# Optimization experiments

Hardware: AMD Instinct MI355X
Metric: run time of the kernel (lower is better)

## Reference

```python
import jax, jax.numpy as jnp
import numpy as np

H = 12        # num attention heads
W = 256       # one-sided window (attention_window // 2)
NEG = -1e9    # additive mask value


def setup_inputs() -> dict:
    key = jax.random.key(0)
    ks = jax.random.split(key, 6)
    B, S, D = 2, 4096, 768
    inp = {
        "hidden_states": jax.random.normal(ks[0], (B, S, D), dtype=jnp.float32),
        "attention_mask": jnp.zeros((B, S), dtype=jnp.float32),
        "Wq": jax.random.normal(ks[1], (D, D), dtype=jnp.float32) * 0.02,
        "bq": jnp.zeros((D,), dtype=jnp.float32),
        "Wk": jax.random.normal(ks[2], (D, D), dtype=jnp.float32) * 0.02,
        "bk": jnp.zeros((D,), dtype=jnp.float32),
        "Wv": jax.random.normal(ks[3], (D, D), dtype=jnp.float32) * 0.02,
        "bv": jnp.zeros((D,), dtype=jnp.float32),
        "Wo": jax.random.normal(ks[4], (D, D), dtype=jnp.float32) * 0.02,
        "bo": jnp.zeros((D,), dtype=jnp.float32),
    }
    return inp


def _sliding_window_attn(hidden_states, attention_mask, Wq, bq, Wk, bk, Wv, bv, Wo, bo):
    B, S, D = hidden_states.shape
    dh = D // H
    b = W                 # chunk size == one-sided window
    nb = S // b           # number of chunks (S must be multiple of W)

    # projections; Longformer scales the query by 1/sqrt(d_head)
    q = (hidden_states @ Wq.T + bq) / jnp.sqrt(jnp.float32(dh))
    k = hidden_states @ Wk.T + bk
    v = hidden_states @ Wv.T + bv

    # [B, H, S, dh]
    q = q.reshape(B, S, H, dh).transpose(0, 2, 1, 3)
    k = k.reshape(B, S, H, dh).transpose(0, 2, 1, 3)
    v = v.reshape(B, S, H, dh).transpose(0, 2, 1, 3)

    # chunk queries: [B, H, nb, b, dh]
    qb = q.reshape(B, H, nb, b, dh)

    # pad K/V by one chunk on each side, gather 3 consecutive chunks per query chunk
    kp = jnp.pad(k, ((0, 0), (0, 0), (b, b), (0, 0)))
    vp = jnp.pad(v, ((0, 0), (0, 0), (b, b), (0, 0)))
    idx = jnp.arange(nb)[:, None] * b + jnp.arange(3 * b)[None, :]  # [nb, 3b] into padded seq
    kw = kp[:, :, idx]  # [B, H, nb, 3b, dh]
    vw = vp[:, :, idx]  # [B, H, nb, 3b, dh]

    # banded scores: [B, H, nb, b, 3b]
    scores = jnp.einsum("bhnqd,bhnkd->bhnqk", qb, kw)

    # band mask: query at local pos qi (global n*b+qi) vs key at local pos ki
    # (global n*b + ki - b); relative offset = ki - b - qi, keep |offset| <= W
    rel = jnp.arange(3 * b)[None, :] - b - jnp.arange(b)[:, None]      # [b, 3b]
    band = jnp.abs(rel) <= W
    # sequence-boundary mask: key global position must lie in [0, S)
    kpos = idx - b                                                      # [nb, 3b]
    inbounds = (kpos >= 0) & (kpos < S)
    valid = band[None, :, :] & inbounds[:, None, :]                     # [nb, b, 3b]

    # key padding bias from attention_mask (wrapper passes attention_mask * -1)
    neg_mask = attention_mask * -1.0                                    # [B, S]
    mp = jnp.pad(neg_mask, ((0, 0), (b, b)))
    key_bias = mp[:, idx]                                               # [B, nb, 3b]

    scores = scores + key_bias[:, None, :, None, :]
    scores = jnp.where(valid[None, None], scores, NEG)

    probs = jax.nn.softmax(scores, axis=-1)
    ctx = jnp.einsum("bhnqk,bhnkd->bhnqd", probs, vw)                   # [B, H, nb, b, dh]
    ctx = ctx.reshape(B, H, S, dh).transpose(0, 2, 1, 3).reshape(B, S, D)

    return ctx @ Wo.T + bo


def reference(hidden_states, attention_mask, Wq, bq, Wk, bk, Wv, bv, Wo, bo):
    return _sliding_window_attn(hidden_states, attention_mask,
                                Wq, bq, Wk, bk, Wv, bv, Wo, bo)
```

## Files before the change

kernel.cpp:

```cpp
#include <hip/hip_runtime.h>
#include <hip/hip_bf16.h>
#include <stdint.h>

#define NH 12
#define DH 64
#define SEQ 4096
#define DM 768
#define NEGV -1e9f
#define LOG2E 1.4426950408889634f
#define QSCALE 0.1803368801111601f

using bf16x8 = __attribute__((ext_vector_type(8))) short;
using f32x4  = __attribute__((ext_vector_type(4))) float;

static __device__ __forceinline__ short f2bf(float f) {
  unsigned u = __builtin_bit_cast(unsigned, f);
  u += 0x7fffu + ((u >> 16) & 1u);
  return (short)(u >> 16);
}

static __device__ __forceinline__ unsigned pack2bf_rnd(float lo, float hi) {
  unsigned a = __builtin_bit_cast(unsigned, lo) + 0x8000u;
  unsigned b = __builtin_bit_cast(unsigned, hi) + 0x8000u;
  return __builtin_amdgcn_perm(b, a, 0x07060302u);
}

static __device__ __forceinline__ void gload16(const void* g, void* l) {
  __builtin_amdgcn_global_load_lds(
      (const __attribute__((address_space(1))) unsigned*)g,
      (__attribute__((address_space(3))) unsigned*)l, 16, 0, 0);
}

static __device__ __forceinline__ f32x4 mfma16(bf16x8 a, bf16x8 b, f32x4 c) {
  return __builtin_amdgcn_mfma_f32_16x16x32_bf16(a, b, c, 0, 0, 0);
}

#define SBAR() __builtin_amdgcn_sched_barrier(0)
#define WAIT8() asm volatile("s_waitcnt vmcnt(8)" ::: "memory")
#define WAIT0() asm volatile("s_waitcnt vmcnt(0)" ::: "memory")
#define HBAR() __builtin_amdgcn_s_barrier()

__global__ __launch_bounds__(256) void cvt_all(
    const float* __restrict__ X, short* __restrict__ Xb,
    const float* __restrict__ Wq, const float* __restrict__ Wk,
    const float* __restrict__ Wv, const float* __restrict__ Wo,
    short* __restrict__ Wqkv, short* __restrict__ Wob) {
  int i = blockIdx.x * 256 + threadIdx.x;
  const int nx = 8192 * 768 / 4;
  if (i < nx) {
    float4 v = ((const float4*)X)[i];
    short4 o; o.x = f2bf(v.x); o.y = f2bf(v.y); o.z = f2bf(v.z); o.w = f2bf(v.w);
    ((short4*)Xb)[i] = o;
    return;
  }
  i -= nx;
  const int n1 = 2304 * 768 / 4;
  if (i < n1) {
    int e = i * 4;
    int row = e / 768;
    const float* src;
    float sc = 1.0f;
    if (row < 768)       { src = Wq + e; sc = QSCALE; }
    else if (row < 1536) { src = Wk + e - 768 * 768; }
    else                 { src = Wv + e - 1536 * 768; }
    float4 v = *(const float4*)src;
    short4 o; o.x = f2bf(v.x * sc); o.y = f2bf(v.y * sc);
    o.z = f2bf(v.z * sc); o.w = f2bf(v.w * sc);
    ((short4*)Wqkv)[i] = o;
  } else {
    int j = i - n1;
    if (j >= 768 * 768 / 4) return;
    float4 v = ((const float4*)Wo)[j];
    short4 o; o.x = f2bf(v.x); o.y = f2bf(v.y); o.z = f2bf(v.z); o.w = f2bf(v.w);
    ((short4*)Wob)[j] = o;
  }
}

#define GEMM_PIPELINE(SM, AG, BG, ACC, LANE, WR, WC)                           \
  {                                                                            \
    const int l15 = (LANE) & 15, gw = (LANE) >> 4;                             \
    const int s_ = (l15 >> 1) & 3;                                             \
    const int NT = 12;                                             \
    auto stage = [&](int t) {                                                  \
      short* ab = (SM) + ((t & 1) << 13);                                      \
      short* bb = (SM) + 16384 + ((t & 1) << 13);                              \
      int kt = t << 6;                                                         \
      gload16((AG) + kt, ab + ldst);                                           \
      gload16((AG) + kt + 32 * 768, ab + ldst + 2048);                         \
      gload16((AG) + kt + 64 * 768, ab + ldst + 4096);                         \
      gload16((AG) + kt + 96 * 768, ab + ldst + 6144);                         \
      gload16((BG) + kt, bb + ldst);                                           \
      gload16((BG) + kt + 32 * 768, bb + ldst + 2048);                         \
      gload16((BG) + kt + 64 * 768, bb + ldst + 4096);                         \
      gload16((BG) + kt + 96 * 768, bb + ldst + 6144);                         \
    };                                                                         \
    auto compute = [&](int t) {                                                \
      const short* ab = (SM) + ((t & 1) << 13);                                \
      const short* bb = (SM) + 16384 + ((t & 1) << 13);                        \
      _Pragma("unroll") for (int kk = 0; kk < 2; ++kk) {                       \
        const int fc = (((kk << 2) + (gw ^ s_)) << 3);                         \
        bf16x8 af[4], bf[4];                                                   \
        _Pragma("unroll") for (int mi = 0; mi < 4; ++mi)                       \
            af[mi] = *(const bf16x8*)(ab + ((WR) + mi * 16 + l15) * 64 + fc);  \
        _Pragma("unroll") for (int ni = 0; ni < 4; ++ni)                       \
            bf[ni] = *(const bf16x8*)(bb + ((WC) + ni * 16 + l15) * 64 + fc);  \
        __builtin_amdgcn_s_setprio(1);                                         \
        _Pragma("unroll") for (int mi = 0; mi < 4; ++mi)                       \
            _Pragma("unroll") for (int ni = 0; ni < 4; ++ni)                   \
                ACC[mi][ni] = mfma16(af[mi], bf[ni], ACC[mi][ni]);             \
        __builtin_amdgcn_s_setprio(0);                                         \
      }                                                                        \
    };                                                                         \
    stage(0); stage(1);                                                        \
    SBAR();                                                                    \
    _Pragma("unroll 1") for (int i = 0; i < NT; ++i) {                         \
      SBAR();                                                                  \
      if (i < NT - 1) { WAIT8(); } else { WAIT0(); }                           \
      HBAR(); SBAR();                                                          \
      compute(i);                                                              \
      SBAR(); HBAR();                                                          \
      if (i + 2 < NT) stage(i + 2);                                            \
    }                                                                          \
  }

__global__ __launch_bounds__(256) void gemm_qkv(
    const short* __restrict__ Xb, const short* __restrict__ Wqkv,
    const float* __restrict__ bq, const float* __restrict__ bk,
    const float* __restrict__ bv,
    short* __restrict__ qO, short* __restrict__ kO, short* __restrict__ vT) {
  __shared__ __align__(16) short sm[32768];
  const int tid = threadIdx.x, lane = tid & 63, wid = tid >> 6;
  const int xcd = blockIdx.x & 7, kk = blockIdx.x >> 3;
  const int m0 = (xcd * 8 + (kk & 7)) * 128;
  const int n0 = (kk >> 3) * 128;
  const int wr = (wid >> 1) * 64, wc = (wid & 1) * 64;
  const int srow = tid >> 3;
  const int scol = (((tid & 7) ^ ((tid >> 4) & 3)) << 3);
  const short* Ag = Xb + (m0 + srow) * 768 + scol;
  const short* Bg = Wqkv + (n0 + srow) * 768 + scol;
  const int ldst = tid * 8;

  const int src = n0 / 768;
  const int nloc = n0 % 768;
  float bias[4];
#pragma unroll
  for (int ni = 0; ni < 4; ++ni) {
    int c = nloc + wc + ni * 16 + (lane & 15);
    bias[ni] = (src == 0) ? bq[c] * QSCALE : (src == 1) ? bk[c] : bv[c];
  }
  WAIT0(); SBAR();

  f32x4 acc[4][4] = {};
  GEMM_PIPELINE(sm, Ag, Bg, acc, lane, wr, wc);

  const int bb = m0 >> 12;
  const int s0 = m0 & (SEQ - 1);
  __syncthreads();
  if (src < 2) {
#pragma unroll
    for (int mi = 0; mi < 4; ++mi)
#pragma unroll
      for (int ni = 0; ni < 4; ++ni) {
        int row = wr + mi * 16 + ((lane >> 4) << 2);
        int col = wc + ni * 16 + (lane & 15);
#pragma unroll
        for (int r = 0; r < 4; ++r)
          sm[(row + r) * 132 + col] = f2bf(acc[mi][ni][r] + bias[ni]);
      }
    __syncthreads();
    short* dst = (src == 0) ? qO : kO;
    for (int u = tid; u < 8192; u += 256) {
      int r = u >> 6, cp = (u & 63) << 1;
      unsigned val = *(const unsigned*)&sm[r * 132 + cp];
      int c = nloc + cp;
      int h = c >> 6, d = c & 63;
      *(unsigned*)&dst[(((bb * NH + h) * SEQ) + s0 + r) * DH + d] = val;
    }
  } else {
#pragma unroll
    for (int mi = 0; mi < 4; ++mi)
#pragma unroll
      for (int ni = 0; ni < 4; ++ni) {
        int row = wr + mi * 16 + ((lane >> 4) << 2);
        int col = wc + ni * 16 + (lane & 15);
        short4 pk;
        pk.x = f2bf(acc[mi][ni][0] + bias[ni]);
        pk.y = f2bf(acc[mi][ni][1] + bias[ni]);
        pk.z = f2bf(acc[mi][ni][2] + bias[ni]);
        pk.w = f2bf(acc[mi][ni][3] + bias[ni]);
        *(short4*)&sm[col * 132 + row] = pk;
      }
    __syncthreads();
    for (int u = tid; u < 8192; u += 256) {
      int cc = u >> 6, rp = (u & 63) << 1;
      unsigned val = *(const unsigned*)&sm[cc * 132 + rp];
      int c = nloc + cc;
      int h = c >> 6, d = c & 63;
      *(unsigned*)&vT[(((bb * NH + h) * DH) + d) * SEQ + s0 + rp] = val;
    }
  }
}

__global__ __launch_bounds__(512, 4) void attn(
    const short* __restrict__ qI, const short* __restrict__ kI,
    const short* __restrict__ vT, const float* __restrict__ amask,
    short* __restrict__ ctx) {
  __shared__ __align__(16) short Ks[128 * 64];
  __shared__ __align__(16) short Vs[64 * 128];
  __shared__ __align__(16) short Ps[8][16 * 132];
  __shared__ __align__(16) float BiasL[768];
  const int tid = threadIdx.x, lane = tid & 63, wid = tid >> 6;
  const int vb_id = (blockIdx.x & 7) * 96 + (blockIdx.x >> 3);
  const int strip = vb_id & 31;
  const int hh = (vb_id >> 5) % 12;
  const int bb = vb_id / 384;
  const int s0 = strip * 128;
  const int n = s0 >> 8;
  const int i0 = s0 & 255;
  const int base = (n - 1) * 256;
  const int bh = bb * NH + hh;
  const int m = lane & 15, hq = lane >> 4;
  const int swz = m & 7;
  const int iw = i0 + (wid << 4);

  const short* qbase = qI + ((size_t)(bh * SEQ) + s0 + (wid << 4)) * DH;
  const bf16x8 aq0 = *(const bf16x8*)(qbase + m * DH + (hq << 3));
  const bf16x8 aq1 = *(const bf16x8*)(qbase + m * DH + 32 + (hq << 3));

  const int kb_s0 = m * 64 + ((hq ^ swz) << 3);
  const int kb_s1 = m * 64 + (((hq + 4) ^ swz) << 3);
  const int vk0 = m * 128 + ((hq ^ swz) << 3);
  const int vk1 = m * 128 + (((hq + 4) ^ swz) << 3);
  const int vk2 = m * 128 + (((hq + 8) ^ swz) << 3);
  const int vk3 = m * 128 + (((hq + 12) ^ swz) << 3);
  short* Pw = Ps[wid];
  const int pwr = m * 132;

  const int e0 = tid * 8, e1 = tid * 8 + 4096;
  const int kj0 = e0 >> 6, kj1 = e1 >> 6;
  const int ksrc0 = kj0 * DH + ((((e0 >> 3) & 7) ^ (kj0 & 7)) << 3);
  const int ksrc1 = kj1 * DH + ((((e1 >> 3) & 7) ^ (kj1 & 7)) << 3);
  const int vd0 = e0 >> 7, vd1 = e1 >> 7;
  const int vsrc0 = vd0 * SEQ + ((((e0 >> 3) & 15) ^ (vd0 & 7)) << 3);
  const int vsrc1 = vd1 * SEQ + ((((e1 >> 3) & 15) ^ (vd1 & 7)) << 3);

  const short* kg0 = kI + (size_t)bh * SEQ * DH;
  const short* vg0 = vT + (size_t)bh * DH * SEQ;

  if (tid < 192) {
    int idx = base + tid * 4;
    idx = idx < 0 ? 0 : (idx > SEQ - 4 ? SEQ - 4 : idx);
    float4 bv = *(const float4*)(amask + bb * SEQ + idx);
    bv.x *= -LOG2E; bv.y *= -LOG2E; bv.z *= -LOG2E; bv.w *= -LOG2E;
    *(float4*)&BiasL[tid * 4] = bv;
  }

  f32x4 acc[4] = {};
  float mrow = -1e30f, lrow = 0.f;

#pragma unroll 1
  for (int c = 0; c < 6; ++c) {
    const int j0 = c << 7;
    const int kpos0 = base + j0;
    if (kpos0 < 0 || kpos0 >= SEQ) continue;
    if (j0 + 127 < i0 || j0 > i0 + 639) continue;

    __syncthreads();
    {
      const short* kb = kg0 + (size_t)kpos0 * DH;
      gload16(kb + ksrc0, (short*)Ks + e0);
      gload16(kb + ksrc1, (short*)Ks + e1);
      const short* vbp = vg0 + kpos0;
      gload16(vbp + vsrc0, (short*)Vs + e0);
      gload16(vbp + vsrc1, (short*)Vs + e1);
    }
    __syncthreads();

    f32x4 sc[8];
    __builtin_amdgcn_s_setprio(1);
#pragma unroll
    for (int jt = 0; jt < 8; ++jt) {
      bf16x8 k0 = *(const bf16x8*)(Ks + jt * 1024 + kb_s0);
      bf16x8 k1 = *(const bf16x8*)(Ks + jt * 1024 + kb_s1);
      f32x4 z = {};
      z = mfma16(k0, aq0, z);
      z = mfma16(k1, aq1, z);
      sc[jt] = z;
    }
    __builtin_amdgcn_s_setprio(0);

    const float* mp = BiasL + j0 + (hq << 2);
    float mn_l = -3e38f;
    const bool interior = (j0 >= iw + 15) && (j0 <= iw + 385);
    if (interior) {
#pragma unroll
      for (int jt = 0; jt < 8; ++jt) {
        float4 b4 = *(const float4*)(mp + jt * 16);
#pragma unroll
        for (int r = 0; r < 4; ++r) {
          float s = sc[jt][r] + (&b4.x)[r];
          sc[jt][r] = s;
          mn_l = fmaxf(mn_l, s);
        }
      }
    } else {
      const int iq = iw + m;
#pragma unroll
      for (int jt = 0; jt < 8; ++jt) {
        float4 b4 = *(const float4*)(mp + jt * 16);
        const int jb = j0 + jt * 16 + (hq << 2);
#pragma unroll
        for (int r = 0; r < 4; ++r) {
          int j = jb + r;
          float s = sc[jt][r] + (&b4.x)[r];
          s = (j >= iq && j <= iq + 512) ? s : NEGV;
          sc[jt][r] = s;
          mn_l = fmaxf(mn_l, s);
        }
      }
    }

    if (__any(mn_l > mrow + 8.0f)) {
      float mn = fmaxf(mrow, mn_l);
      mn = fmaxf(mn, __shfl_xor(mn, 16));
      mn = fmaxf(mn, __shfl_xor(mn, 32));
      const float scl = exp2f(mrow - mn);
      mrow = mn;
      lrow *= scl;
      const float s0r = __shfl(scl, (hq << 2) + 0);
      const float s1r = __shfl(scl, (hq << 2) + 1);
      const float s2r = __shfl(scl, (hq << 2) + 2);
      const float s3r = __shfl(scl, (hq << 2) + 3);
#pragma unroll
      for (int nt = 0; nt < 4; ++nt) {
        acc[nt][0] *= s0r; acc[nt][1] *= s1r;
        acc[nt][2] *= s2r; acc[nt][3] *= s3r;
      }
    }

    float l0 = 0.f;
#pragma unroll
    for (int jt = 0; jt < 8; ++jt) {
      float p0 = exp2f(sc[jt][0] - mrow);
      float p1 = exp2f(sc[jt][1] - mrow);
      float p2 = exp2f(sc[jt][2] - mrow);
      float p3 = exp2f(sc[jt][3] - mrow);
      l0 += (p0 + p1) + (p2 + p3);
      uint2 u;
      u.x = pack2bf_rnd(p0, p1);
      u.y = pack2bf_rnd(p2, p3);
      *(uint2*)(Pw + pwr + jt * 16 + (hq << 2)) = u;
    }
    lrow += l0;

    asm volatile("s_waitcnt lgkmcnt(0)" ::: "memory");
    __builtin_amdgcn_sched_barrier(0);

    __builtin_amdgcn_s_setprio(1);
#pragma unroll
    for (int ks = 0; ks < 4; ++ks) {
      bf16x8 pa = *(const bf16x8*)(Pw + pwr + ks * 32 + (hq << 3));
      const int vkk = (ks == 0) ? vk0 : (ks == 1) ? vk1 : (ks == 2) ? vk2 : vk3;
#pragma unroll
      for (int nt = 0; nt < 4; ++nt) {
        bf16x8 vv = *(const bf16x8*)(Vs + nt * 2048 + vkk);
        acc[nt] = mfma16(pa, vv, acc[nt]);
      }
    }
    __builtin_amdgcn_s_setprio(0);
  }

  lrow += __shfl_xor(lrow, 16);
  lrow += __shfl_xor(lrow, 32);
  const float inv = 1.0f / lrow;
  const float i0r = __shfl(inv, (hq << 2) + 0);
  const float i1r = __shfl(inv, (hq << 2) + 1);
  const float i2r = __shfl(inv, (hq << 2) + 2);
  const float i3r = __shfl(inv, (hq << 2) + 3);
#pragma unroll
  for (int nt = 0; nt < 4; ++nt) {
    Pw[((hq << 2) + 0) * 72 + nt * 16 + m] = f2bf(acc[nt][0] * i0r);
    Pw[((hq << 2) + 1) * 72 + nt * 16 + m] = f2bf(acc[nt][1] * i1r);
    Pw[((hq << 2) + 2) * 72 + nt * 16 + m] = f2bf(acc[nt][2] * i2r);
    Pw[((hq << 2) + 3) * 72 + nt * 16 + m] = f2bf(acc[nt][3] * i3r);
  }
  asm volatile("s_waitcnt lgkmcnt(0)" ::: "memory");
  __builtin_amdgcn_sched_barrier(0);
#pragma unroll
  for (int it = 0; it < 2; ++it) {
    int row = it * 8 + (lane >> 3);
    bf16x8 val = *(const bf16x8*)(Pw + row * 72 + ((lane & 7) << 3));
    *(bf16x8*)(ctx + ((size_t)(bb * SEQ) + s0 + (wid << 4) + row) * DM +
               hh * DH + ((lane & 7) << 3)) = val;
  }
}

__global__ __launch_bounds__(256) void gemm_out(
    const short* __restrict__ Cb, const short* __restrict__ Wob,
    const float* __restrict__ bo, float* __restrict__ out) {
  __shared__ __align__(16) short sm[32768];
  const int tid = threadIdx.x, lane = tid & 63, wid = tid >> 6;
  const int xcd = blockIdx.x & 7, kk = blockIdx.x >> 3;
  const int m0 = (xcd * 8 + (kk & 7)) * 128;
  const int n0 = (kk >> 3) * 128;
  const int wr = (wid >> 1) * 64, wc = (wid & 1) * 64;
  const int srow = tid >> 3;
  const int scol = (((tid & 7) ^ ((tid >> 4) & 3)) << 3);
  const short* Ag = Cb + (m0 + srow) * 768 + scol;
  const short* Bg = Wob + (n0 + srow) * 768 + scol;
  const int ldst = tid * 8;

  float bias[4];
#pragma unroll
  for (int ni = 0; ni < 4; ++ni)
    bias[ni] = bo[n0 + wc + ni * 16 + (lane & 15)];
  WAIT0(); SBAR();

  f32x4 acc[4][4] = {};
  GEMM_PIPELINE(sm, Ag, Bg, acc, lane, wr, wc);

#pragma unroll
  for (int mi = 0; mi < 4; ++mi)
#pragma unroll
    for (int ni = 0; ni < 4; ++ni) {
      int row = m0 + wr + mi * 16 + ((lane >> 4) << 2);
      int col = n0 + wc + ni * 16 + (lane & 15);
#pragma unroll
      for (int r = 0; r < 4; ++r)
        out[(row + r) * DM + col] = acc[mi][ni][r] + bias[ni];
    }
}

extern "C" void kernel_launch(void* const* d_in, const int* in_sizes, int n_in,
                              void* d_out, int out_size, void* d_ws, size_t ws_size,
                              hipStream_t stream) {
  (void)in_sizes; (void)n_in; (void)out_size; (void)ws_size;
  const float* hs    = (const float*)d_in[0];
  const float* amask = (const float*)d_in[1];
  const float* Wq = (const float*)d_in[2];
  const float* bq = (const float*)d_in[3];
  const float* Wk = (const float*)d_in[4];
  const float* bk = (const float*)d_in[5];
  const float* Wv = (const float*)d_in[6];
  const float* bv = (const float*)d_in[7];
  const float* Wo = (const float*)d_in[8];
  const float* bo = (const float*)d_in[9];
  float* out = (float*)d_out;
  char* ws = (char*)d_ws;
  short* Xb   = (short*)(ws);
  short* Wqkv = (short*)(ws + 12582912);
  short* Wob  = (short*)(ws + 16121856);
  short* qB   = (short*)(ws + 17301504);
  short* kB   = (short*)(ws + 29884416);
  short* vTB  = (short*)(ws + 42467328);
  short* ctx  = Xb;

  cvt_all<<<dim3(8448), dim3(256), 0, stream>>>(hs, Xb, Wq, Wk, Wv, Wo, Wqkv, Wob);
  gemm_qkv<<<dim3(1152), dim3(256), 0, stream>>>(Xb, Wqkv, bq, bk, bv, qB, kB, vTB);
  attn<<<dim3(768), dim3(512), 0, stream>>>(qB, kB, vTB, amask, ctx);
  gemm_out<<<dim3(384), dim3(256), 0, stream>>>(ctx, Wob, bo, out);
}
```

Before: 123.6 us.

## Enlarge QKV GEMM block tile to 256x128 with 512 threads

```diff
diff --git a/kernel.cpp b/kernel.cpp
--- a/kernel.cpp
+++ b/kernel.cpp
@@ -37,6 +37,7 @@
 
 #define SBAR() __builtin_amdgcn_sched_barrier(0)
 #define WAIT8() asm volatile("s_waitcnt vmcnt(8)" ::: "memory")
+#define WAIT6() asm volatile("s_waitcnt vmcnt(6)" ::: "memory")
 #define WAIT0() asm volatile("s_waitcnt vmcnt(0)" ::: "memory")
 #define HBAR() __builtin_amdgcn_s_barrier()
 
@@ -123,80 +124,149 @@
     }                                                                          \
   }
 
-__global__ __launch_bounds__(256) void gemm_qkv(
+__global__ __launch_bounds__(512) void gemm_qkv(
     const short* __restrict__ Xb, const short* __restrict__ Wqkv,
     const float* __restrict__ bq, const float* __restrict__ bk,
     const float* __restrict__ bv,
     short* __restrict__ qO, short* __restrict__ kO, short* __restrict__ vT) {
-  __shared__ __align__(16) short sm[32768];
+  __shared__ __align__(16) short sm[49152];
   const int tid = threadIdx.x, lane = tid & 63, wid = tid >> 6;
   const int xcd = blockIdx.x & 7, kk = blockIdx.x >> 3;
-  const int m0 = (xcd * 8 + (kk & 7)) * 128;
-  const int n0 = (kk >> 3) * 128;
-  const int wr = (wid >> 1) * 64, wc = (wid & 1) * 64;
-  const int srow = tid >> 3;
-  const int scol = (((tid & 7) ^ ((tid >> 4) & 3)) << 3);
-  const short* Ag = Xb + (m0 + srow) * 768 + scol;
-  const short* Bg = Wqkv + (n0 + srow) * 768 + scol;
+  const int m0 = (xcd * 4 + (kk & 3)) * 256;
+  const int n0 = (kk >> 2) * 128;
+  const int wrow = (wid >> 1) * 64, wcol = (wid & 1) * 64;
+  const int l15 = lane & 15, gw = lane >> 4;
+  const int s_ = (l15 >> 1) & 3;
   const int ldst = tid * 8;
+
+  int aoff[4], boff[2];
+#pragma unroll
+  for (int p = 0; p < 4; ++p) {
+    int e = p * 4096 + ldst;
+    int row = e >> 6;
+    int gs = ((e >> 3) & 7) ^ ((row >> 1) & 3);
+    aoff[p] = row * 768 + (gs << 3);
+  }
+#pragma unroll
+  for (int p = 0; p < 2; ++p) {
+    int e = p * 4096 + ldst;
+    int row = e >> 6;
+    int gs = ((e >> 3) & 7) ^ ((row >> 1) & 3);
+    boff[p] = row * 768 + (gs << 3);
+  }
+  const short* Ag = Xb + (size_t)m0 * 768;
+  const short* Bg = Wqkv + (size_t)n0 * 768;
 
   const int src = n0 / 768;
   const int nloc = n0 % 768;
   float bias[4];
 #pragma unroll
   for (int ni = 0; ni < 4; ++ni) {
-    int c = nloc + wc + ni * 16 + (lane & 15);
+    int c = nloc + wcol + ni * 16 + l15;
     bias[ni] = (src == 0) ? bq[c] * QSCALE : (src == 1) ? bk[c] : bv[c];
   }
   WAIT0(); SBAR();
 
+  auto stage = [&](int t) {
+    short* ab = sm + ((t & 1) << 14);
+    short* bb = sm + 32768 + ((t & 1) << 13);
+    int kt = t << 6;
+#pragma unroll
+    for (int p = 0; p < 4; ++p) gload16(Ag + aoff[p] + kt, ab + p * 4096 + ldst);
+#pragma unroll
+    for (int p = 0; p < 2; ++p) gload16(Bg + boff[p] + kt, bb + p * 4096 + ldst);
+  };
   f32x4 acc[4][4] = {};
-  GEMM_PIPELINE(sm, Ag, Bg, acc, lane, wr, wc);
-
-  const int bb = m0 >> 12;
+  auto compute = [&](int t) {
+    const short* ab = sm + ((t & 1) << 14);
+    const short* bb = sm + 32768 + ((t & 1) << 13);
+#pragma unroll
+    for (int kk2 = 0; kk2 < 2; ++kk2) {
+      const int fc = (((kk2 << 2) + (gw ^ s_)) << 3);
+      bf16x8 af[4], bf[4];
+#pragma unroll
+      for (int mi = 0; mi < 4; ++mi)
+        af[mi] = *(const bf16x8*)(ab + (wrow + mi * 16 + l15) * 64 + fc);
+#pragma unroll
+      for (int ni = 0; ni < 4; ++ni)
+        bf[ni] = *(const bf16x8*)(bb + (wcol + ni * 16 + l15) * 64 + fc);
+      __builtin_amdgcn_s_setprio(1);
+#pragma unroll
+      for (int mi = 0; mi < 4; ++mi)
+#pragma unroll
+        for (int ni = 0; ni < 4; ++ni)
+          acc[mi][ni] = mfma16(af[mi], bf[ni], acc[mi][ni]);
+      __builtin_amdgcn_s_setprio(0);
+    }
+  };
+
+  stage(0); stage(1);
+  SBAR();
+#pragma unroll 1
+  for (int i = 0; i < 12; ++i) {
+    SBAR();
+    if (i < 11) { WAIT6(); } else { WAIT0(); }
+    HBAR(); SBAR();
+    compute(i);
+    SBAR(); HBAR();
+    if (i + 2 < 12) stage(i + 2);
+  }
+
+  const int bb_ = m0 >> 12;
   const int s0 = m0 & (SEQ - 1);
-  __syncthreads();
   if (src < 2) {
-#pragma unroll
-    for (int mi = 0; mi < 4; ++mi)
-#pragma unroll
-      for (int ni = 0; ni < 4; ++ni) {
-        int row = wr + mi * 16 + ((lane >> 4) << 2);
-        int col = wc + ni * 16 + (lane & 15);
-#pragma unroll
-        for (int r = 0; r < 4; ++r)
-          sm[(row + r) * 132 + col] = f2bf(acc[mi][ni][r] + bias[ni]);
-      }
-    __syncthreads();
     short* dst = (src == 0) ? qO : kO;
-    for (int u = tid; u < 8192; u += 256) {
-      int r = u >> 6, cp = (u & 63) << 1;
-      unsigned val = *(const unsigned*)&sm[r * 132 + cp];
-      int c = nloc + cp;
-      int h = c >> 6, d = c & 63;
-      *(unsigned*)&dst[(((bb * NH + h) * SEQ) + s0 + r) * DH + d] = val;
+#pragma unroll 1
+    for (int h = 0; h < 2; ++h) {
+      __syncthreads();
+      if ((wrow >> 7) == h) {
+#pragma unroll
+        for (int mi = 0; mi < 4; ++mi)
+#pragma unroll
+          for (int ni = 0; ni < 4; ++ni) {
+            int row = (wrow & 127) + mi * 16 + ((lane >> 4) << 2);
+            int col = wcol + ni * 16 + l15;
+#pragma unroll
+            for (int r = 0; r < 4; ++r)
+              sm[(row + r) * 132 + col] = f2bf(acc[mi][ni][r] + bias[ni]);
+          }
+      }
+      __syncthreads();
+      for (int u = tid; u < 8192; u += 512) {
+        int r = u >> 6, cp = (u & 63) << 1;
+        unsigned val = *(const unsigned*)&sm[r * 132 + cp];
+        int c = nloc + cp;
+        int hh = c >> 6, d = c & 63;
+        *(unsigned*)&dst[(((bb_ * NH + hh) * SEQ) + s0 + h * 128 + r) * DH + d] = val;
+      }
     }
   } else {
-#pragma unroll
-    for (int mi = 0; mi < 4; ++mi)
-#pragma unroll
-      for (int ni = 0; ni < 4; ++ni) {
-        int row = wr + mi * 16 + ((lane >> 4) << 2);
-        int col = wc + ni * 16 + (lane & 15);
-        short4 pk;
-        pk.x = f2bf(acc[mi][ni][0] + bias[ni]);
-        pk.y = f2bf(acc[mi][ni][1] + bias[ni]);
-        pk.z = f2bf(acc[mi][ni][2] + bias[ni]);
-        pk.w = f2bf(acc[mi][ni][3] + bias[ni]);
-        *(short4*)&sm[col * 132 + row] = pk;
-      }
-    __syncthreads();
-    for (int u = tid; u < 8192; u += 256) {
-      int cc = u >> 6, rp = (u & 63) << 1;
-      unsigned val = *(const unsigned*)&sm[cc * 132 + rp];
-      int c = nloc + cc;
-      int h = c >> 6, d = c & 63;
-      *(unsigned*)&vT[(((bb * NH + h) * DH) + d) * SEQ + s0 + rp] = val;
+#pragma unroll 1
+    for (int h = 0; h < 2; ++h) {
+      __syncthreads();
+      if ((wrow >> 7) == h) {
+#pragma unroll
+        for (int mi = 0; mi < 4; ++mi)
+#pragma unroll
+          for (int ni = 0; ni < 4; ++ni) {
+            int row = (wrow & 127) + mi * 16 + ((lane >> 4) << 2);
+            int col = wcol + ni * 16 + l15;
+            short4 pk;
+            pk.x = f2bf(acc[mi][ni][0] + bias[ni]);
+            pk.y = f2bf(acc[mi][ni][1] + bias[ni]);
+            pk.z = f2bf(acc[mi][ni][2] + bias[ni]);
+            pk.w = f2bf(acc[mi][ni][3] + bias[ni]);
+            *(short4*)&sm[col * 132 + row] = pk;
+          }
+      }
+      __syncthreads();
+      for (int u = tid; u < 8192; u += 512) {
+        int cc = u >> 6, rp = (u & 63) << 1;
+        unsigned val = *(const unsigned*)&sm[cc * 132 + rp];
+        int c = nloc + cc;
+        int hh = c >> 6, d = c & 63;
+        *(unsigned*)&vT[(((bb_ * NH + hh) * DH) + d) * SEQ + s0 + h * 128 + rp] = val;
+      }
     }
   }
 }
@@ -456,7 +526,7 @@
   short* ctx  = Xb;
 
   cvt_all<<<dim3(8448), dim3(256), 0, stream>>>(hs, Xb, Wq, Wk, Wv, Wo, Wqkv, Wob);
-  gemm_qkv<<<dim3(1152), dim3(256), 0, stream>>>(Xb, Wqkv, bq, bk, bv, qB, kB, vTB);
+  gemm_qkv<<<dim3(576), dim3(512), 0, stream>>>(Xb, Wqkv, bq, bk, bv, qB, kB, vTB);
   attn<<<dim3(768), dim3(512), 0, stream>>>(qB, kB, vTB, amask, ctx);
   gemm_out<<<dim3(384), dim3(256), 0, stream>>>(ctx, Wob, bo, out);
 }
```

New measurement: 136.5 us. 10.4% more time.

## Run QKV GEMM with 512 threads and a 32x64 per-wave tile

Applied to the files above, without the earlier changes.

```diff
diff --git a/kernel.cpp b/kernel.cpp
--- a/kernel.cpp
+++ b/kernel.cpp
@@ -37,6 +37,7 @@
 
 #define SBAR() __builtin_amdgcn_sched_barrier(0)
 #define WAIT8() asm volatile("s_waitcnt vmcnt(8)" ::: "memory")
+#define WAIT4() asm volatile("s_waitcnt vmcnt(4)" ::: "memory")
 #define WAIT0() asm volatile("s_waitcnt vmcnt(0)" ::: "memory")
 #define HBAR() __builtin_amdgcn_s_barrier()
 
@@ -123,7 +124,7 @@
     }                                                                          \
   }
 
-__global__ __launch_bounds__(256) void gemm_qkv(
+__global__ __launch_bounds__(512) void gemm_qkv(
     const short* __restrict__ Xb, const short* __restrict__ Wqkv,
     const float* __restrict__ bq, const float* __restrict__ bk,
     const float* __restrict__ bv,
@@ -133,56 +134,106 @@
   const int xcd = blockIdx.x & 7, kk = blockIdx.x >> 3;
   const int m0 = (xcd * 8 + (kk & 7)) * 128;
   const int n0 = (kk >> 3) * 128;
-  const int wr = (wid >> 1) * 64, wc = (wid & 1) * 64;
-  const int srow = tid >> 3;
-  const int scol = (((tid & 7) ^ ((tid >> 4) & 3)) << 3);
-  const short* Ag = Xb + (m0 + srow) * 768 + scol;
-  const short* Bg = Wqkv + (n0 + srow) * 768 + scol;
+  const int wr = (wid >> 1) * 32, wc = (wid & 1) * 64;
+  const int l15 = lane & 15, gw = lane >> 4;
+  const int s_ = (l15 >> 1) & 3;
   const int ldst = tid * 8;
+
+  int off0, off1;
+  {
+    int e = ldst;            int row = e >> 6;
+    off0 = row * 768 + (((((e >> 3) & 7) ^ ((row >> 1) & 3))) << 3);
+    e = 4096 + ldst;         row = e >> 6;
+    off1 = row * 768 + (((((e >> 3) & 7) ^ ((row >> 1) & 3))) << 3);
+  }
+  const short* Ag = Xb + (size_t)m0 * 768;
+  const short* Bg = Wqkv + (size_t)n0 * 768;
 
   const int src = n0 / 768;
   const int nloc = n0 % 768;
   float bias[4];
 #pragma unroll
   for (int ni = 0; ni < 4; ++ni) {
-    int c = nloc + wc + ni * 16 + (lane & 15);
+    int c = nloc + wc + ni * 16 + l15;
     bias[ni] = (src == 0) ? bq[c] * QSCALE : (src == 1) ? bk[c] : bv[c];
   }
   WAIT0(); SBAR();
 
-  f32x4 acc[4][4] = {};
-  GEMM_PIPELINE(sm, Ag, Bg, acc, lane, wr, wc);
-
-  const int bb = m0 >> 12;
+  auto stage = [&](int t) {
+    short* ab = sm + ((t & 1) << 13);
+    short* bb = sm + 16384 + ((t & 1) << 13);
+    int kt = t << 6;
+    gload16(Ag + off0 + kt, ab + ldst);
+    gload16(Ag + off1 + kt, ab + 4096 + ldst);
+    gload16(Bg + off0 + kt, bb + ldst);
+    gload16(Bg + off1 + kt, bb + 4096 + ldst);
+  };
+  f32x4 acc[2][4] = {};
+  auto compute = [&](int t) {
+    const short* ab = sm + ((t & 1) << 13);
+    const short* bb = sm + 16384 + ((t & 1) << 13);
+#pragma unroll
+    for (int kk2 = 0; kk2 < 2; ++kk2) {
+      const int fc = (((kk2 << 2) + (gw ^ s_)) << 3);
+      bf16x8 af[2], bf[4];
+#pragma unroll
+      for (int mi = 0; mi < 2; ++mi)
+        af[mi] = *(const bf16x8*)(ab + (wr + mi * 16 + l15) * 64 + fc);
+#pragma unroll
+      for (int ni = 0; ni < 4; ++ni)
+        bf[ni] = *(const bf16x8*)(bb + (wc + ni * 16 + l15) * 64 + fc);
+      __builtin_amdgcn_s_setprio(1);
+#pragma unroll
+      for (int mi = 0; mi < 2; ++mi)
+#pragma unroll
+        for (int ni = 0; ni < 4; ++ni)
+          acc[mi][ni] = mfma16(af[mi], bf[ni], acc[mi][ni]);
+      __builtin_amdgcn_s_setprio(0);
+    }
+  };
+
+  stage(0); stage(1);
+  SBAR();
+#pragma unroll 1
+  for (int i = 0; i < 12; ++i) {
+    SBAR();
+    if (i < 11) { WAIT4(); } else { WAIT0(); }
+    HBAR(); SBAR();
+    compute(i);
+    SBAR(); HBAR();
+    if (i + 2 < 12) stage(i + 2);
+  }
+
+  const int bb_ = m0 >> 12;
   const int s0 = m0 & (SEQ - 1);
   __syncthreads();
   if (src < 2) {
 #pragma unroll
-    for (int mi = 0; mi < 4; ++mi)
+    for (int mi = 0; mi < 2; ++mi)
 #pragma unroll
       for (int ni = 0; ni < 4; ++ni) {
         int row = wr + mi * 16 + ((lane >> 4) << 2);
-        int col = wc + ni * 16 + (lane & 15);
+        int col = wc + ni * 16 + l15;
 #pragma unroll
         for (int r = 0; r < 4; ++r)
           sm[(row + r) * 132 + col] = f2bf(acc[mi][ni][r] + bias[ni]);
       }
     __syncthreads();
     short* dst = (src == 0) ? qO : kO;
-    for (int u = tid; u < 8192; u += 256) {
+    for (int u = tid; u < 8192; u += 512) {
       int r = u >> 6, cp = (u & 63) << 1;
       unsigned val = *(const unsigned*)&sm[r * 132 + cp];
       int c = nloc + cp;
       int h = c >> 6, d = c & 63;
-      *(unsigned*)&dst[(((bb * NH + h) * SEQ) + s0 + r) * DH + d] = val;
+      *(unsigned*)&dst[(((bb_ * NH + h) * SEQ) + s0 + r) * DH + d] = val;
     }
   } else {
 #pragma unroll
-    for (int mi = 0; mi < 4; ++mi)
+    for (int mi = 0; mi < 2; ++mi)
 #pragma unroll
       for (int ni = 0; ni < 4; ++ni) {
         int row = wr + mi * 16 + ((lane >> 4) << 2);
-        int col = wc + ni * 16 + (lane & 15);
+        int col = wc + ni * 16 + l15;
         short4 pk;
         pk.x = f2bf(acc[mi][ni][0] + bias[ni]);
         pk.y = f2bf(acc[mi][ni][1] + bias[ni]);
@@ -191,12 +242,12 @@
         *(short4*)&sm[col * 132 + row] = pk;
       }
     __syncthreads();
-    for (int u = tid; u < 8192; u += 256) {
+    for (int u = tid; u < 8192; u += 512) {
       int cc = u >> 6, rp = (u & 63) << 1;
       unsigned val = *(const unsigned*)&sm[cc * 132 + rp];
       int c = nloc + cc;
       int h = c >> 6, d = c & 63;
-      *(unsigned*)&vT[(((bb * NH + h) * DH) + d) * SEQ + s0 + rp] = val;
+      *(unsigned*)&vT[(((bb_ * NH + h) * DH) + d) * SEQ + s0 + rp] = val;
     }
   }
 }
@@ -456,7 +507,7 @@
   short* ctx  = Xb;
 
   cvt_all<<<dim3(8448), dim3(256), 0, stream>>>(hs, Xb, Wq, Wk, Wv, Wo, Wqkv, Wob);
-  gemm_qkv<<<dim3(1152), dim3(256), 0, stream>>>(Xb, Wqkv, bq, bk, bv, qB, kB, vTB);
+  gemm_qkv<<<dim3(1152), dim3(512), 0, stream>>>(Xb, Wqkv, bq, bk, bv, qB, kB, vTB);
   attn<<<dim3(768), dim3(512), 0, stream>>>(qB, kB, vTB, amask, ctx);
   gemm_out<<<dim3(384), dim3(256), 0, stream>>>(ctx, Wob, bo, out);
 }
```

After: 121.8 us. Within noise of the previous version (-1.5%).
